# Performance work log

Measured on AMD Instinct MI355X. Metric: run time of the kernel, lower is better.

## Reference

```python
import jax, jax.numpy as jnp
import numpy as np

N = 40000
E = 200000
D = 32
NUM_BANDS = 3
ORDER = 4
EPS = 1e-8
LN_EPS = 1e-5


def setup_inputs() -> dict:
    key = jax.random.key(0)
    ks = jax.random.split(key, 20)
    h = jax.random.normal(ks[0], (N, D), dtype=jnp.float32)
    Q = jax.random.normal(ks[1], (E, D, D), dtype=jnp.float32) / jnp.sqrt(jnp.float32(D))
    edge_index = jax.random.randint(ks[2], (2, E), 0, N, dtype=jnp.int32)
    coeffs = jnp.ones((NUM_BANDS, ORDER + 1), dtype=jnp.float32) / (ORDER + 1)
    s = 1.0 / np.sqrt(D)
    proj_W = jax.random.uniform(ks[3], (NUM_BANDS, D, D), minval=-s, maxval=s, dtype=jnp.float32)
    proj_b = jax.random.uniform(ks[4], (NUM_BANDS, D), minval=-s, maxval=s, dtype=jnp.float32)
    proj_g = jnp.ones((NUM_BANDS, D), dtype=jnp.float32)
    proj_beta = jnp.zeros((NUM_BANDS, D), dtype=jnp.float32)
    s3 = 1.0 / np.sqrt(NUM_BANDS * D)
    fus_W1 = jax.random.uniform(ks[5], (NUM_BANDS * D, D), minval=-s3, maxval=s3, dtype=jnp.float32)
    fus_b1 = jax.random.uniform(ks[6], (D,), minval=-s3, maxval=s3, dtype=jnp.float32)
    fus_g = jnp.ones((D,), dtype=jnp.float32)
    fus_beta = jnp.zeros((D,), dtype=jnp.float32)
    fus_W2 = jax.random.uniform(ks[7], (D, D), minval=-s, maxval=s, dtype=jnp.float32)
    fus_b2 = jax.random.uniform(ks[8], (D,), minval=-s, maxval=s, dtype=jnp.float32)
    return {"h": h, "Q": Q, "edge_index": edge_index, "coeffs": coeffs,
            "proj_W": proj_W, "proj_b": proj_b, "proj_g": proj_g, "proj_beta": proj_beta,
            "fus_W1": fus_W1, "fus_b1": fus_b1, "fus_g": fus_g, "fus_beta": fus_beta,
            "fus_W2": fus_W2, "fus_b2": fus_b2}


def _layer_norm(x, g, b):
    mu = x.mean(-1, keepdims=True)
    var = x.var(-1, keepdims=True)  # biased, as torch LayerNorm
    return (x - mu) / jnp.sqrt(var + LN_EPS) * g + b


def reference(h, Q, edge_index, coeffs, proj_W, proj_b, proj_g, proj_beta,
              fus_W1, fus_b1, fus_g, fus_beta, fus_W2, fus_b2):
    row, col = edge_index[0], edge_index[1]
    n = h.shape[0]
    ones_e = jnp.ones(row.shape[0], dtype=h.dtype)
    deg = (jax.ops.segment_sum(ones_e, row, num_segments=n)
           + jax.ops.segment_sum(ones_e, col, num_segments=n))  # [N]

    def matvec(x):
        # gather -> per-edge DxD bmm -> scatter_add; diag via degree
        Qh = jnp.einsum('eij,ej->ei', Q, x[col])          # [E, D]
        off = jax.ops.segment_sum(Qh, row, num_segments=n)  # [N, D]
        return deg[:, None] * x - off

    # power iteration for lambda_max (5 iters, fixed key for determinism)
    v = jax.random.normal(jax.random.key(42), h.shape, dtype=h.dtype)
    v = v / jnp.linalg.norm(v)
    lam = jnp.array(1.0, dtype=h.dtype)
    for _ in range(5):
        Lv = matvec(v)
        lam = (v * Lv).sum() / ((v * v).sum() + EPS)
        v = Lv / (jnp.linalg.norm(Lv) + EPS)
    lam = jnp.maximum(lam, 1.0)

    def L_tilde(x):
        return 2.0 / (lam + EPS) * matvec(x) - x

    bands = []
    for b_idx in range(NUM_BANDS):
        w = jax.nn.softmax(coeffs[b_idx])
        T_prev = h
        T_curr = L_tilde(h)
        res = w[0] * T_prev + w[1] * T_curr
        for k in range(2, ORDER + 1):
            T_next = 2.0 * L_tilde(T_curr) - T_prev
            res = res + w[k] * T_next
            T_prev, T_curr = T_curr, T_next
        p = jax.nn.silu(_layer_norm(res @ proj_W[b_idx] + proj_b[b_idx],
                                    proj_g[b_idx], proj_beta[b_idx]))
        bands.append(p)

    cat = jnp.concatenate(bands, axis=-1)  # [N, 3D]
    fused = jax.nn.silu(_layer_norm(cat @ fus_W1 + fus_b1, fus_g, fus_beta)) @ fus_W2 + fus_b2
    return h + fused
```

## Files before the change

### kernel.cpp

```cpp
#include <hip/hip_runtime.h>
#include <hip/hip_fp16.h>
#include <math.h>

#define NN 40000
#define EE 200000
#define DD 32
#define ND (NN * DD)
#define LNEPS 1e-5f

typedef float    fv4 __attribute__((ext_vector_type(4)));
typedef unsigned uv4 __attribute__((ext_vector_type(4)));

#define SLOT_S1    0
#define SLOT_S2    32
#define SLOT_ALPHA 48

__device__ __forceinline__ void threefry2x32(unsigned k0, unsigned k1,
                                             unsigned x0, unsigned x1,
                                             unsigned& o0, unsigned& o1) {
  const unsigned k2 = k0 ^ k1 ^ 0x1BD11BDAu;
  unsigned v0 = x0 + k0, v1 = x1 + k1;
#define TF_ROUND(r) { v0 += v1; v1 = (v1 << (r)) | (v1 >> (32 - (r))); v1 ^= v0; }
  TF_ROUND(13) TF_ROUND(15) TF_ROUND(26) TF_ROUND(6)
  v0 += k1; v1 += k2 + 1u;
  TF_ROUND(17) TF_ROUND(29) TF_ROUND(16) TF_ROUND(24)
  v0 += k2; v1 += k0 + 2u;
  TF_ROUND(13) TF_ROUND(15) TF_ROUND(26) TF_ROUND(6)
  v0 += k0; v1 += k1 + 3u;
  TF_ROUND(17) TF_ROUND(29) TF_ROUND(16) TF_ROUND(24)
  v0 += k1; v1 += k2 + 4u;
  TF_ROUND(13) TF_ROUND(15) TF_ROUND(26) TF_ROUND(6)
  v0 += k2; v1 += k0 + 5u;
#undef TF_ROUND
  o0 = v0; o1 = v1;
}

__device__ __forceinline__ float wave64_sum(float x) {
  for (int o = 32; o > 0; o >>= 1) x += __shfl_xor(x, o, 64);
  return x;
}
__device__ __forceinline__ float g32_sum(float x) {
  for (int o = 16; o > 0; o >>= 1) x += __shfl_xor(x, o, 32);
  return x;
}

__global__ void k_deg(const int* __restrict__ ei, float* __restrict__ deg) {
  int e = blockIdx.x * 256 + threadIdx.x;
  if (e < EE) {
    atomicAdd(deg + ei[e], 1.0f);
    atomicAdd(deg + ei[EE + e], 1.0f);
  }
}

__global__ void k_genv(float* __restrict__ v) {
  int i = blockIdx.x * 256 + threadIdx.x;
  unsigned o0, o1;
  threefry2x32(0u, 42u, 0u, (unsigned)i, o0, o1);
  unsigned bits = o1;
  float f = __uint_as_float((bits >> 9) | 0x3f800000u) - 1.0f;
  const float lo = -0.99999994f;
  float u = fmaxf(lo, f * 2.0f + lo);
  v[i] = 1.41421354f * erfinvf(u);
}

__global__ void k_pre(const float* __restrict__ x, const float* __restrict__ xprev,
                      const float* __restrict__ deg, const float* __restrict__ scal,
                      float* __restrict__ out, int mode) {
  int i = blockIdx.x * 256 + threadIdx.x;
  float d = deg[i >> 5];
  float xi = x[i];
  if (mode == 0)       out[i] = d * xi;
  else if (mode == 1)  out[i] = scal[SLOT_ALPHA] * d * xi - xi;
  else                 out[i] = 2.0f * scal[SLOT_ALPHA] * d * xi - 2.0f * xi - xprev[i];
}

__device__ __forceinline__ int clamp8(float q) {
  int v = (int)rintf(q);
  return v < -127 ? -127 : (v > 127 ? 127 : v);
}
__device__ __forceinline__ unsigned pack4v(fv4 q, float inv) {
  int q0 = clamp8(q.x * inv), q1 = clamp8(q.y * inv),
      q2 = clamp8(q.z * inv), q3 = clamp8(q.w * inv);
  return (q0 & 255) | ((q1 & 255) << 8) | ((q2 & 255) << 16) | ((q3 & 255) << 24);
}
__device__ __forceinline__ void dp4(unsigned u, fv4 xv, float& acc) {
  acc = fmaf((float)(signed char)(u),        xv.x, acc);
  acc = fmaf((float)(signed char)(u >> 8),   xv.y, acc);
  acc = fmaf((float)(signed char)(u >> 16),  xv.z, acc);
  acc = fmaf((float)(signed char)(u >> 24),  xv.w, acc);
}

__global__ __launch_bounds__(256) void k_matvec_cvt(const float* __restrict__ x,
                                                    const float* __restrict__ Q,
                                                    const int* __restrict__ ei,
                                                    float* __restrict__ out,
                                                    char* __restrict__ Qi8,
                                                    __half* __restrict__ Qs) {
  const int slot = threadIdx.x >> 5;
  const int lane = threadIdx.x & 31;
  const int e = blockIdx.x * 8 + slot;
  const int row = ei[e];
  const int col = ei[EE + e];
  const fv4* __restrict__ x4 = (const fv4*)(x + (size_t)col * DD);
  fv4 xr[8];
#pragma unroll
  for (int k = 0; k < 8; ++k) xr[k] = x4[k];
  const fv4* __restrict__ q4 =
      (const fv4*)(Q + (size_t)e * (DD * DD) + (size_t)lane * DD);
  fv4 qf[8];
#pragma unroll
  for (int k = 0; k < 8; ++k) qf[k] = __builtin_nontemporal_load(q4 + k);
  float acc = 0.0f;
#pragma unroll
  for (int k = 0; k < 8; ++k) {
    acc = fmaf(qf[k].x, xr[k].x, acc);
    acc = fmaf(qf[k].y, xr[k].y, acc);
    acc = fmaf(qf[k].z, xr[k].z, acc);
    acc = fmaf(qf[k].w, xr[k].w, acc);
  }
  float m = 0.0f;
#pragma unroll
  for (int k = 0; k < 8; ++k) {
    m = fmaxf(m, fmaxf(fmaxf(fabsf(qf[k].x), fabsf(qf[k].y)),
                       fmaxf(fabsf(qf[k].z), fabsf(qf[k].w))));
  }
  __half sh = __float2half(m * (1.0f / 127.0f));
  float s = __half2float(sh);
  float inv = (s > 0.0f) ? 1.0f / s : 0.0f;
  uv4 pa, pb;
  pa.x = pack4v(qf[0], inv);
  pa.y = pack4v(qf[1], inv);
  pa.z = pack4v(qf[2], inv);
  pa.w = pack4v(qf[3], inv);
  pb.x = pack4v(qf[4], inv);
  pb.y = pack4v(qf[5], inv);
  pb.z = pack4v(qf[6], inv);
  pb.w = pack4v(qf[7], inv);
  uv4* __restrict__ qs = (uv4*)(Qi8 + (size_t)e * (DD * DD) + (size_t)lane * DD);
  __builtin_nontemporal_store(pa, qs);
  __builtin_nontemporal_store(pb, qs + 1);
  Qs[e * DD + lane] = sh;
  atomicAdd(out + (size_t)row * DD + lane, -acc);
}

__global__ __launch_bounds__(256) void k_matvec_i8(const float* __restrict__ x,
                                                   const char* __restrict__ Qi8,
                                                   const __half* __restrict__ Qs,
                                                   const int* __restrict__ ei,
                                                   float* __restrict__ out,
                                                   const float* __restrict__ scal,
                                                   int use_alpha, float smul) {
  const int slot = threadIdx.x >> 5;
  const int lane = threadIdx.x & 31;
  const int e = blockIdx.x * 8 + slot;
  const float factor = use_alpha ? scal[SLOT_ALPHA] * smul : smul;
  const int row = ei[e];
  const int col = ei[EE + e];
  const fv4* __restrict__ x4 = (const fv4*)(x + (size_t)col * DD);
  fv4 xr[8];
#pragma unroll
  for (int k = 0; k < 8; ++k) xr[k] = x4[k];
  const uv4* __restrict__ q8 =
      (const uv4*)(Qi8 + (size_t)e * (DD * DD) + (size_t)lane * DD);
  uv4 pa = __builtin_nontemporal_load(q8);
  uv4 pb = __builtin_nontemporal_load(q8 + 1);
  float s = __half2float(Qs[e * DD + lane]);
  float acc = 0.0f;
  dp4(pa.x, xr[0], acc); dp4(pa.y, xr[1], acc);
  dp4(pa.z, xr[2], acc); dp4(pa.w, xr[3], acc);
  dp4(pb.x, xr[4], acc); dp4(pb.y, xr[5], acc);
  dp4(pb.z, xr[6], acc); dp4(pb.w, xr[7], acc);
  atomicAdd(out + (size_t)row * DD + lane, -factor * s * acc);
}

__global__ __launch_bounds__(256) void k_matvec(const float* __restrict__ x,
                                                const float* __restrict__ Q,
                                                const int* __restrict__ ei,
                                                float* __restrict__ out,
                                                const float* __restrict__ scal,
                                                int use_alpha, float smul) {
  const int slot = threadIdx.x >> 5;
  const int lane = threadIdx.x & 31;
  const int e = blockIdx.x * 8 + slot;
  const float factor = use_alpha ? scal[SLOT_ALPHA] * smul : smul;
  const int row = ei[e];
  const int col = ei[EE + e];
  const fv4* __restrict__ x4 = (const fv4*)(x + (size_t)col * DD);
  fv4 xr[8];
#pragma unroll
  for (int k = 0; k < 8; ++k) xr[k] = x4[k];
  const fv4* __restrict__ q4 =
      (const fv4*)(Q + (size_t)e * (DD * DD) + (size_t)lane * DD);
  float acc = 0.0f;
#pragma unroll
  for (int k = 0; k < 8; ++k) {
    fv4 q = q4[k];
    acc = fmaf(q.x, xr[k].x, acc);
    acc = fmaf(q.y, xr[k].y, acc);
    acc = fmaf(q.z, xr[k].z, acc);
    acc = fmaf(q.w, xr[k].w, acc);
  }
  atomicAdd(out + (size_t)row * DD + lane, -factor * acc);
}

#define DOT_BLOCKS 640
__global__ void k_dots(const float* __restrict__ u4, const float* __restrict__ u5,
                       float* __restrict__ scal) {
  float s1 = 0.0f, s2 = 0.0f;
  for (int i = blockIdx.x * 256 + threadIdx.x; i < ND; i += DOT_BLOCKS * 256) {
    float a = u4[i], b = u5[i];
    s1 = fmaf(a, b, s1);
    s2 = fmaf(a, a, s2);
  }
  s1 = wave64_sum(s1);
  s2 = wave64_sum(s2);
  __shared__ float ls1[4], ls2[4];
  int w = threadIdx.x >> 6;
  if ((threadIdx.x & 63) == 0) { ls1[w] = s1; ls2[w] = s2; }
  __syncthreads();
  if (threadIdx.x == 0) {
    atomicAdd(scal + SLOT_S1, ls1[0] + ls1[1] + ls1[2] + ls1[3]);
    atomicAdd(scal + SLOT_S2, ls2[0] + ls2[1] + ls2[2] + ls2[3]);
  }
}

__global__ void k_alpha(float* __restrict__ scal) {
  float lam = scal[SLOT_S1] / scal[SLOT_S2] / (1.0f + 1e-8f);
  lam = fmaxf(lam, 1.0f);
  scal[SLOT_ALPHA] = 2.0f / (lam + 1e-8f);
}

__global__ __launch_bounds__(256) void k_fuse(
    const float* __restrict__ h,
    const float* __restrict__ T1, const float* __restrict__ T2,
    const float* __restrict__ T3, const float* __restrict__ T4,
    const float* __restrict__ coeffs,
    const float* __restrict__ projW, const float* __restrict__ projb,
    const float* __restrict__ projg, const float* __restrict__ projbeta,
    const float* __restrict__ fusW1, const float* __restrict__ fusb1,
    const float* __restrict__ fusg, const float* __restrict__ fusbeta,
    const float* __restrict__ fusW2, const float* __restrict__ fusb2,
    float* __restrict__ out) {
  __shared__ float s_res[8][3][DD];
  __shared__ float s_p[8][3 * DD];
  __shared__ float s_s[8][DD];
  const int slot = threadIdx.x >> 5;
  const int lane = threadIdx.x & 31;
  const int n = blockIdx.x * 8 + slot;

  float w[3][5];
#pragma unroll
  for (int b = 0; b < 3; ++b) {
    float m = -1e30f;
#pragma unroll
    for (int k = 0; k < 5; ++k) m = fmaxf(m, coeffs[b * 5 + k]);
    float s = 0.0f;
#pragma unroll
    for (int k = 0; k < 5; ++k) { w[b][k] = expf(coeffs[b * 5 + k] - m); s += w[b][k]; }
#pragma unroll
    for (int k = 0; k < 5; ++k) w[b][k] /= s;
  }

  const int idx = n * DD + lane;
  float hd = h[idx], t1 = T1[idx], t2 = T2[idx], t3 = T3[idx], t4 = T4[idx];
#pragma unroll
  for (int b = 0; b < 3; ++b)
    s_res[slot][b][lane] =
        w[b][0] * hd + w[b][1] * t1 + w[b][2] * t2 + w[b][3] * t3 + w[b][4] * t4;
  __syncthreads();

#pragma unroll
  for (int b = 0; b < 3; ++b) {
    float y = projb[b * DD + lane];
#pragma unroll
    for (int j = 0; j < DD; ++j)
      y = fmaf(s_res[slot][b][j], projW[(b * DD + j) * DD + lane], y);
    float mu = g32_sum(y) * (1.0f / DD);
    float d = y - mu;
    float var = g32_sum(d * d) * (1.0f / DD);
    float z = d * rsqrtf(var + LNEPS) * projg[b * DD + lane] + projbeta[b * DD + lane];
    float pb = z / (1.0f + expf(-z));
    s_p[slot][b * DD + lane] = pb;
  }
  __syncthreads();

  float y = fusb1[lane];
#pragma unroll
  for (int j = 0; j < 3 * DD; ++j)
    y = fmaf(s_p[slot][j], fusW1[j * DD + lane], y);
  float mu = g32_sum(y) * (1.0f / DD);
  float d = y - mu;
  float var = g32_sum(d * d) * (1.0f / DD);
  float z = d * rsqrtf(var + LNEPS) * fusg[lane] + fusbeta[lane];
  float sv = z / (1.0f + expf(-z));
  s_s[slot][lane] = sv;
  __syncthreads();

  float o = fusb2[lane];
#pragma unroll
  for (int j = 0; j < DD; ++j)
    o = fmaf(s_s[slot][j], fusW2[j * DD + lane], o);
  out[idx] = hd + o;
}

extern "C" void kernel_launch(void* const* d_in, const int* in_sizes, int n_in,
                              void* d_out, int out_size, void* d_ws, size_t ws_size,
                              hipStream_t stream) {
  (void)in_sizes; (void)n_in; (void)out_size;
  const float* h        = (const float*)d_in[0];
  const float* Q        = (const float*)d_in[1];
  const int*   ei       = (const int*)d_in[2];
  const float* coeffs   = (const float*)d_in[3];
  const float* projW    = (const float*)d_in[4];
  const float* projb    = (const float*)d_in[5];
  const float* projg    = (const float*)d_in[6];
  const float* projbeta = (const float*)d_in[7];
  const float* fusW1    = (const float*)d_in[8];
  const float* fusb1    = (const float*)d_in[9];
  const float* fusg     = (const float*)d_in[10];
  const float* fusbeta  = (const float*)d_in[11];
  const float* fusW2    = (const float*)d_in[12];
  const float* fusb2    = (const float*)d_in[13];
  float* out = (float*)d_out;

  const size_t qi_bytes = (size_t)EE * DD * DD;
  const size_t qs_bytes = (size_t)EE * DD * sizeof(__half);
  const size_t f32_elems = 6u * ND + NN + 64;
  const bool use_i8 = ws_size >= qi_bytes + qs_bytes + f32_elems * sizeof(float);

  char*   Qi8 = (char*)d_ws;
  __half* Qs  = (__half*)((char*)d_ws + qi_bytes);
  float* base = use_i8 ? (float*)((char*)d_ws + qi_bytes + qs_bytes) : (float*)d_ws;
  float* uA   = base;
  float* uB   = uA + ND;
  float* T1   = uB + ND;
  float* T2   = T1 + ND;
  float* T3   = T2 + ND;
  float* T4   = T3 + ND;
  float* deg  = T4 + ND;
  float* scal = deg + NN;

  (void)hipMemsetAsync(deg, 0, (NN + 64) * sizeof(float), stream);

  k_deg<<<(EE + 255) / 256, 256, 0, stream>>>(ei, deg);
  k_genv<<<ND / 256, 256, 0, stream>>>(uA);

  float* cur = uA;
  float* nxt = uB;
  for (int it = 0; it < 5; ++it) {
    k_pre<<<ND / 256, 256, 0, stream>>>(cur, nullptr, deg, scal, nxt, 0);
    if (it == 0 && use_i8)
      k_matvec_cvt<<<EE / 8, 256, 0, stream>>>(cur, Q, ei, nxt, Qi8, Qs);
    else if (use_i8)
      k_matvec_i8<<<EE / 8, 256, 0, stream>>>(cur, Qi8, Qs, ei, nxt, scal, 0, 1.0f);
    else
      k_matvec<<<EE / 8, 256, 0, stream>>>(cur, Q, ei, nxt, scal, 0, 1.0f);
    float* t = cur; cur = nxt; nxt = t;
  }
  k_dots<<<DOT_BLOCKS, 256, 0, stream>>>(nxt, cur, scal);
  k_alpha<<<1, 1, 0, stream>>>(scal);

  const float* xin[4]   = {h, T1, T2, T3};
  const float* prevs[4] = {nullptr, h, T1, T2};
  float* touts[4]       = {T1, T2, T3, T4};
  for (int k = 0; k < 4; ++k) {
    k_pre<<<ND / 256, 256, 0, stream>>>(xin[k], prevs[k], deg, scal, touts[k],
                                        k == 0 ? 1 : 2);
    float smul = (k == 0) ? 1.0f : 2.0f;
    if (use_i8)
      k_matvec_i8<<<EE / 8, 256, 0, stream>>>(xin[k], Qi8, Qs, ei, touts[k], scal, 1, smul);
    else
      k_matvec<<<EE / 8, 256, 0, stream>>>(xin[k], Q, ei, touts[k], scal, 1, smul);
  }

  k_fuse<<<NN / 8, 256, 0, stream>>>(h, T1, T2, T3, T4, coeffs,
                                     projW, projb, projg, projbeta,
                                     fusW1, fusb1, fusg, fusbeta,
                                     fusW2, fusb2, out);
}
```

Measured before the change: 1.039 ms.

## Sort edges into CSR by row and replace atomic scatter with row gather

Builds a per-row histogram and prefix scan, then reorders the int8-quantized Q blocks and column indices into CSR order during the one-time conversion. Each matvec becomes a row-parallel gather kernel that accumulates locally and fuses the diagonal/Chebyshev pre-step, removing the separate k_pre pass and the float atomics. The cost is an extra scan kernel and a first power iteration that no longer overlaps conversion with compute. Rows with many edges serialize in one 32-lane group, so load imbalance is a risk.

```diff
diff --git a/kernel.cpp b/kernel.cpp
--- a/kernel.cpp
+++ b/kernel.cpp
@@ -44,12 +44,40 @@
   return x;
 }
 
-__global__ void k_deg(const int* __restrict__ ei, float* __restrict__ deg) {
+__global__ void k_deg(const int* __restrict__ ei, float* __restrict__ deg,
+                      int* __restrict__ hist) {
   int e = blockIdx.x * 256 + threadIdx.x;
   if (e < EE) {
-    atomicAdd(deg + ei[e], 1.0f);
+    int r = ei[e];
+    atomicAdd(deg + r, 1.0f);
     atomicAdd(deg + ei[EE + e], 1.0f);
-  }
+    atomicAdd(hist + r, 1);
+  }
+}
+
+__global__ __launch_bounds__(1024) void k_scan(const int* __restrict__ hist,
+                                               int* __restrict__ row_start,
+                                               int* __restrict__ cursor) {
+  __shared__ int part[1024];
+  const int t = threadIdx.x;
+  const int base = t * 40;
+  int s = 0;
+  for (int i = base; i < base + 40 && i < NN; ++i) s += hist[i];
+  part[t] = s;
+  __syncthreads();
+  for (int off = 1; off < 1024; off <<= 1) {
+    int v = (t >= off) ? part[t - off] : 0;
+    __syncthreads();
+    part[t] += v;
+    __syncthreads();
+  }
+  int ex = (t == 0) ? 0 : part[t - 1];
+  for (int i = base; i < base + 40 && i < NN; ++i) {
+    row_start[i] = ex;
+    cursor[i] = ex;
+    ex += hist[i];
+  }
+  if (t == 0) row_start[NN] = EE;
 }
 
 __global__ void k_genv(float* __restrict__ v) {
@@ -63,6 +91,106 @@
   v[i] = 1.41421354f * erfinvf(u);
 }
 
+__device__ __forceinline__ int clamp8(float q) {
+  int v = (int)rintf(q);
+  return v < -127 ? -127 : (v > 127 ? 127 : v);
+}
+__device__ __forceinline__ unsigned pack4v(fv4 q, float inv) {
+  int q0 = clamp8(q.x * inv), q1 = clamp8(q.y * inv),
+      q2 = clamp8(q.z * inv), q3 = clamp8(q.w * inv);
+  return (q0 & 255) | ((q1 & 255) << 8) | ((q2 & 255) << 16) | ((q3 & 255) << 24);
+}
+__device__ __forceinline__ void dp4(unsigned u, fv4 xv, float& acc) {
+  acc = fmaf((float)(signed char)(u),        xv.x, acc);
+  acc = fmaf((float)(signed char)(u >> 8),   xv.y, acc);
+  acc = fmaf((float)(signed char)(u >> 16),  xv.z, acc);
+  acc = fmaf((float)(signed char)(u >> 24),  xv.w, acc);
+}
+
+__global__ __launch_bounds__(256) void k_cvt(const float* __restrict__ Q,
+                                             const int* __restrict__ ei,
+                                             int* __restrict__ cursor,
+                                             char* __restrict__ Qi8,
+                                             __half* __restrict__ Qs,
+                                             int* __restrict__ cols) {
+  const int slot = threadIdx.x >> 5;
+  const int lane = threadIdx.x & 31;
+  const int e = blockIdx.x * 8 + slot;
+  const int row = ei[e];
+  const int col = ei[EE + e];
+  int pos = 0;
+  if (lane == 0) pos = atomicAdd(cursor + row, 1);
+  pos = __shfl(pos, 0, 32);
+  const fv4* __restrict__ q4 =
+      (const fv4*)(Q + (size_t)e * (DD * DD) + (size_t)lane * DD);
+  fv4 qf[8];
+#pragma unroll
+  for (int k = 0; k < 8; ++k) qf[k] = __builtin_nontemporal_load(q4 + k);
+  float m = 0.0f;
+#pragma unroll
+  for (int k = 0; k < 8; ++k) {
+    m = fmaxf(m, fmaxf(fmaxf(fabsf(qf[k].x), fabsf(qf[k].y)),
+                       fmaxf(fabsf(qf[k].z), fabsf(qf[k].w))));
+  }
+  __half sh = __float2half(m * (1.0f / 127.0f));
+  float s = __half2float(sh);
+  float inv = (s > 0.0f) ? 1.0f / s : 0.0f;
+  uv4 pa, pb;
+  pa.x = pack4v(qf[0], inv); pa.y = pack4v(qf[1], inv);
+  pa.z = pack4v(qf[2], inv); pa.w = pack4v(qf[3], inv);
+  pb.x = pack4v(qf[4], inv); pb.y = pack4v(qf[5], inv);
+  pb.z = pack4v(qf[6], inv); pb.w = pack4v(qf[7], inv);
+  uv4* __restrict__ qs = (uv4*)(Qi8 + (size_t)pos * (DD * DD) + (size_t)lane * DD);
+  qs[0] = pa;
+  qs[1] = pb;
+  Qs[pos * DD + lane] = sh;
+  if (lane == 0) cols[pos] = col;
+}
+
+__global__ __launch_bounds__(256) void k_gather(const float* __restrict__ x,
+                                                const float* __restrict__ xprev,
+                                                const char* __restrict__ Qi8,
+                                                const __half* __restrict__ Qs,
+                                                const int* __restrict__ cols,
+                                                const int* __restrict__ row_start,
+                                                const float* __restrict__ deg,
+                                                const float* __restrict__ scal,
+                                                float* __restrict__ out, int mode) {
+  const int slot = threadIdx.x >> 5;
+  const int lane = threadIdx.x & 31;
+  const int r = blockIdx.x * 8 + slot;
+  const int beg = row_start[r];
+  const int end = row_start[r + 1];
+  float off_acc = 0.0f;
+  for (int p = beg; p < end; ++p) {
+    const int col = cols[p];
+    const fv4* __restrict__ x4 = (const fv4*)(x + (size_t)col * DD);
+    fv4 xr[8];
+#pragma unroll
+    for (int k = 0; k < 8; ++k) xr[k] = x4[k];
+    const uv4* __restrict__ q8 =
+        (const uv4*)(Qi8 + (size_t)p * (DD * DD) + (size_t)lane * DD);
+    uv4 pa = q8[0];
+    uv4 pb = q8[1];
+    float s = __half2float(Qs[p * DD + lane]);
+    float d = 0.0f;
+    dp4(pa.x, xr[0], d); dp4(pa.y, xr[1], d);
+    dp4(pa.z, xr[2], d); dp4(pa.w, xr[3], d);
+    dp4(pb.x, xr[4], d); dp4(pb.y, xr[5], d);
+    dp4(pb.z, xr[6], d); dp4(pb.w, xr[7], d);
+    off_acc = fmaf(s, d, off_acc);
+  }
+  const size_t idx = (size_t)r * DD + lane;
+  const float xi = x[idx];
+  const float dv = deg[r];
+  float o;
+  if (mode == 0)      o = dv * xi - off_acc;
+  else if (mode == 1) o = scal[SLOT_ALPHA] * (dv * xi - off_acc) - xi;
+  else                o = 2.0f * scal[SLOT_ALPHA] * (dv * xi - off_acc)
+                          - 2.0f * xi - xprev[idx];
+  out[idx] = o;
+}
+
 __global__ void k_pre(const float* __restrict__ x, const float* __restrict__ xprev,
                       const float* __restrict__ deg, const float* __restrict__ scal,
                       float* __restrict__ out, int mode) {
@@ -72,105 +200,6 @@
   if (mode == 0)       out[i] = d * xi;
   else if (mode == 1)  out[i] = scal[SLOT_ALPHA] * d * xi - xi;
   else                 out[i] = 2.0f * scal[SLOT_ALPHA] * d * xi - 2.0f * xi - xprev[i];
-}
-
-__device__ __forceinline__ int clamp8(float q) {
-  int v = (int)rintf(q);
-  return v < -127 ? -127 : (v > 127 ? 127 : v);
-}
-__device__ __forceinline__ unsigned pack4v(fv4 q, float inv) {
-  int q0 = clamp8(q.x * inv), q1 = clamp8(q.y * inv),
-      q2 = clamp8(q.z * inv), q3 = clamp8(q.w * inv);
-  return (q0 & 255) | ((q1 & 255) << 8) | ((q2 & 255) << 16) | ((q3 & 255) << 24);
-}
-__device__ __forceinline__ void dp4(unsigned u, fv4 xv, float& acc) {
-  acc = fmaf((float)(signed char)(u),        xv.x, acc);
-  acc = fmaf((float)(signed char)(u >> 8),   xv.y, acc);
-  acc = fmaf((float)(signed char)(u >> 16),  xv.z, acc);
-  acc = fmaf((float)(signed char)(u >> 24),  xv.w, acc);
-}
-
-__global__ __launch_bounds__(256) void k_matvec_cvt(const float* __restrict__ x,
-                                                    const float* __restrict__ Q,
-                                                    const int* __restrict__ ei,
-                                                    float* __restrict__ out,
-                                                    char* __restrict__ Qi8,
-                                                    __half* __restrict__ Qs) {
-  const int slot = threadIdx.x >> 5;
-  const int lane = threadIdx.x & 31;
-  const int e = blockIdx.x * 8 + slot;
-  const int row = ei[e];
-  const int col = ei[EE + e];
-  const fv4* __restrict__ x4 = (const fv4*)(x + (size_t)col * DD);
-  fv4 xr[8];
-#pragma unroll
-  for (int k = 0; k < 8; ++k) xr[k] = x4[k];
-  const fv4* __restrict__ q4 =
-      (const fv4*)(Q + (size_t)e * (DD * DD) + (size_t)lane * DD);
-  fv4 qf[8];
-#pragma unroll
-  for (int k = 0; k < 8; ++k) qf[k] = __builtin_nontemporal_load(q4 + k);
-  float acc = 0.0f;
-#pragma unroll
-  for (int k = 0; k < 8; ++k) {
-    acc = fmaf(qf[k].x, xr[k].x, acc);
-    acc = fmaf(qf[k].y, xr[k].y, acc);
-    acc = fmaf(qf[k].z, xr[k].z, acc);
-    acc = fmaf(qf[k].w, xr[k].w, acc);
-  }
-  float m = 0.0f;
-#pragma unroll
-  for (int k = 0; k < 8; ++k) {
-    m = fmaxf(m, fmaxf(fmaxf(fabsf(qf[k].x), fabsf(qf[k].y)),
-                       fmaxf(fabsf(qf[k].z), fabsf(qf[k].w))));
-  }
-  __half sh = __float2half(m * (1.0f / 127.0f));
-  float s = __half2float(sh);
-  float inv = (s > 0.0f) ? 1.0f / s : 0.0f;
-  uv4 pa, pb;
-  pa.x = pack4v(qf[0], inv);
-  pa.y = pack4v(qf[1], inv);
-  pa.z = pack4v(qf[2], inv);
-  pa.w = pack4v(qf[3], inv);
-  pb.x = pack4v(qf[4], inv);
-  pb.y = pack4v(qf[5], inv);
-  pb.z = pack4v(qf[6], inv);
-  pb.w = pack4v(qf[7], inv);
-  uv4* __restrict__ qs = (uv4*)(Qi8 + (size_t)e * (DD * DD) + (size_t)lane * DD);
-  __builtin_nontemporal_store(pa, qs);
-  __builtin_nontemporal_store(pb, qs + 1);
-  Qs[e * DD + lane] = sh;
-  atomicAdd(out + (size_t)row * DD + lane, -acc);
-}
-
-__global__ __launch_bounds__(256) void k_matvec_i8(const float* __restrict__ x,
-                                                   const char* __restrict__ Qi8,
-                                                   const __half* __restrict__ Qs,
-                                                   const int* __restrict__ ei,
-                                                   float* __restrict__ out,
-                                                   const float* __restrict__ scal,
-                                                   int use_alpha, float smul) {
-  const int slot = threadIdx.x >> 5;
-  const int lane = threadIdx.x & 31;
-  const int e = blockIdx.x * 8 + slot;
-  const float factor = use_alpha ? scal[SLOT_ALPHA] * smul : smul;
-  const int row = ei[e];
-  const int col = ei[EE + e];
-  const fv4* __restrict__ x4 = (const fv4*)(x + (size_t)col * DD);
-  fv4 xr[8];
-#pragma unroll
-  for (int k = 0; k < 8; ++k) xr[k] = x4[k];
-  const uv4* __restrict__ q8 =
-      (const uv4*)(Qi8 + (size_t)e * (DD * DD) + (size_t)lane * DD);
-  uv4 pa = __builtin_nontemporal_load(q8);
-  uv4 pb = __builtin_nontemporal_load(q8 + 1);
-  float s = __half2float(Qs[e * DD + lane]);
-  float acc = 0.0f;
-  dp4(pa.x, xr[0], acc); dp4(pa.y, xr[1], acc);
-  dp4(pa.z, xr[2], acc); dp4(pa.w, xr[3], acc);
-  dp4(pb.x, xr[4], acc); dp4(pb.y, xr[5], acc);
-  dp4(pb.z, xr[6], acc); dp4(pb.w, xr[7], acc);
-  atomicAdd(out + (size_t)row * DD + lane, -factor * s * acc);
 }
 
 __global__ __launch_bounds__(256) void k_matvec(const float* __restrict__ x,
@@ -323,14 +352,23 @@
   const float* fusb2    = (const float*)d_in[13];
   float* out = (float*)d_out;
 
-  const size_t qi_bytes = (size_t)EE * DD * DD;
-  const size_t qs_bytes = (size_t)EE * DD * sizeof(__half);
-  const size_t f32_elems = 6u * ND + NN + 64;
-  const bool use_i8 = ws_size >= qi_bytes + qs_bytes + f32_elems * sizeof(float);
+  const size_t qi_bytes  = (size_t)EE * DD * DD;
+  const size_t qs_bytes  = (size_t)EE * DD * sizeof(__half);
+  const size_t col_bytes = (size_t)EE * sizeof(int);
+  const size_t idx_bytes = (size_t)(3 * NN + 2) * sizeof(int);
+  const size_t f32_elems = 6u * (size_t)ND + NN + 64;
+  const size_t need = qi_bytes + qs_bytes + col_bytes + idx_bytes +
+                      f32_elems * sizeof(float) + 256;
+  const bool fast = ws_size >= need;
 
   char*   Qi8 = (char*)d_ws;
   __half* Qs  = (__half*)((char*)d_ws + qi_bytes);
-  float* base = use_i8 ? (float*)((char*)d_ws + qi_bytes + qs_bytes) : (float*)d_ws;
+  int*  cols      = (int*)((char*)d_ws + qi_bytes + qs_bytes);
+  int*  row_start = cols + EE;
+  int*  cursor    = row_start + NN + 1;
+  float* base = fast
+      ? (float*)((char*)d_ws + ((qi_bytes + qs_bytes + col_bytes + idx_bytes + 255) & ~(size_t)255))
+      : (float*)d_ws;
   float* uA   = base;
   float* uB   = uA + ND;
   float* T1   = uB + ND;
@@ -339,38 +377,54 @@
   float* T4   = T3 + ND;
   float* deg  = T4 + ND;
   float* scal = deg + NN;
-
-  (void)hipMemsetAsync(deg, 0, (NN + 64) * sizeof(float), stream);
-
-  k_deg<<<(EE + 255) / 256, 256, 0, stream>>>(ei, deg);
+  int*   hist = (int*)(scal + 64);
+
+  (void)hipMemsetAsync(deg, 0, (2 * NN + 64) * sizeof(float), stream);
+
+  k_deg<<<(EE + 255) / 256, 256, 0, stream>>>(ei, deg, hist);
   k_genv<<<ND / 256, 256, 0, stream>>>(uA);
 
-  float* cur = uA;
-  float* nxt = uB;
-  for (int it = 0; it < 5; ++it) {
-    k_pre<<<ND / 256, 256, 0, stream>>>(cur, nullptr, deg, scal, nxt, 0);
-    if (it == 0 && use_i8)
-      k_matvec_cvt<<<EE / 8, 256, 0, stream>>>(cur, Q, ei, nxt, Qi8, Qs);
-    else if (use_i8)
-      k_matvec_i8<<<EE / 8, 256, 0, stream>>>(cur, Qi8, Qs, ei, nxt, scal, 0, 1.0f);
-    else
+  if (fast) {
+    k_scan<<<1, 1024, 0, stream>>>(hist, row_start, cursor);
+    k_cvt<<<EE / 8, 256, 0, stream>>>(Q, ei, cursor, Qi8, Qs, cols);
+
+    float* cur = uA;
+    float* nxt = uB;
+    for (int it = 0; it < 5; ++it) {
+      k_gather<<<NN / 8, 256, 0, stream>>>(cur, nullptr, Qi8, Qs, cols,
+                                           row_start, deg, scal, nxt, 0);
+      float* t = cur; cur = nxt; nxt = t;
+    }
+    k_dots<<<DOT_BLOCKS, 256, 0, stream>>>(nxt, cur, scal);
+    k_alpha<<<1, 1, 0, stream>>>(scal);
+
+    const float* xin[4]   = {h, T1, T2, T3};
+    const float* prevs[4] = {nullptr, h, T1, T2};
+    float* touts[4]       = {T1, T2, T3, T4};
+    for (int k = 0; k < 4; ++k) {
+      k_gather<<<NN / 8, 256, 0, stream>>>(xin[k], prevs[k], Qi8, Qs, cols,
+                                           row_start, deg, scal, touts[k],
+                                           k == 0 ? 1 : 2);
+    }
+  } else {
+    float* cur = uA;
+    float* nxt = uB;
+    for (int it = 0; it < 5; ++it) {
+      k_pre<<<ND / 256, 256, 0, stream>>>(cur, nullptr, deg, scal, nxt, 0);
       k_matvec<<<EE / 8, 256, 0, stream>>>(cur, Q, ei, nxt, scal, 0, 1.0f);
-    float* t = cur; cur = nxt; nxt = t;
-  }
-  k_dots<<<DOT_BLOCKS, 256, 0, stream>>>(nxt, cur, scal);
-  k_alpha<<<1, 1, 0, stream>>>(scal);
-
-  const float* xin[4]   = {h, T1, T2, T3};
-  const float* prevs[4] = {nullptr, h, T1, T2};
-  float* touts[4]       = {T1, T2, T3, T4};
-  for (int k = 0; k < 4; ++k) {
-    k_pre<<<ND / 256, 256, 0, stream>>>(xin[k], prevs[k], deg, scal, touts[k],
-                                        k == 0 ? 1 : 2);
-    float smul = (k == 0) ? 1.0f : 2.0f;
-    if (use_i8)
-      k_matvec_i8<<<EE / 8, 256, 0, stream>>>(xin[k], Qi8, Qs, ei, touts[k], scal, 1, smul);
-    else
-      k_matvec<<<EE / 8, 256, 0, stream>>>(xin[k], Q, ei, touts[k], scal, 1, smul);
+      float* t = cur; cur = nxt; nxt = t;
+    }
+    k_dots<<<DOT_BLOCKS, 256, 0, stream>>>(nxt, cur, scal);
+    k_alpha<<<1, 1, 0, stream>>>(scal);
+    const float* xin[4]   = {h, T1, T2, T3};
+    const float* prevs[4] = {nullptr, h, T1, T2};
+    float* touts[4]       = {T1, T2, T3, T4};
+    for (int k = 0; k < 4; ++k) {
+      k_pre<<<ND / 256, 256, 0, stream>>>(xin[k], prevs[k], deg, scal, touts[k],
+                                          k == 0 ? 1 : 2);
+      k_matvec<<<EE / 8, 256, 0, stream>>>(xin[k], Q, ei, touts[k], scal, 1,
+                                           k == 0 ? 1.0f : 2.0f);
+    }
   }
 
   k_fuse<<<NN / 8, 256, 0, stream>>>(h, T1, T2, T3, T4, coeffs,
```

Result: no change. 1.037 ms (-0.2%).
